# Optimization experiments

Hardware: AMD Instinct MI355X
Metric: run time of the kernel (lower is better)

The kernel has to match this reference:

```python
import jax, jax.numpy as jnp
import numpy as np

IN_F, OUT_F, RANK = 4096, 4096, 16
SCALING = 1.0  # alpha defaults to rank -> alpha/rank == 1.0


def setup_inputs() -> dict:
    key = jax.random.key(0)
    k1, k2, k3, k4 = jax.random.split(key, 4)
    x = jax.random.normal(k1, (4, 2048, IN_F), dtype=jnp.float32)
    base_weight = jax.random.normal(k2, (OUT_F, IN_F), dtype=jnp.float32)
    U = jax.random.normal(k3, (OUT_F, RANK), dtype=jnp.float32)
    s = jnp.ones((RANK,), dtype=jnp.float32)
    V = jax.random.normal(k4, (IN_F, RANK), dtype=jnp.float32)
    return {"x": x, "base_weight": base_weight, "U": U, "s": s, "V": V}


def reference(x, base_weight, U, s, V):
    # delta_weight = scaling * (U * s) @ V^T, shape (out, in)
    delta_w = SCALING * jnp.einsum('or,ir->oi', U * s[None, :], V)
    adapted = base_weight + delta_w
    # x @ adapted^T : (..., in) -> (..., out)
    return jnp.einsum('bsi,oi->bso', x, adapted)
```

## Files before the change

### kernel.cpp

```cpp
#include <hip/hip_runtime.h>


#define IN_F   4096
#define OUT_F  4096
#define RANK   16
#define M_ROWS 8192
#define BM 128
#define BN 128
#define BK 32

typedef _Float16 f16x8 __attribute__((ext_vector_type(8)));
typedef _Float16 f16x4 __attribute__((ext_vector_type(4)));
typedef float    f32x4 __attribute__((ext_vector_type(4)));

__device__ __forceinline__ void async16(const void* gp, void* lp) {
  __builtin_amdgcn_global_load_lds(
      (const __attribute__((address_space(1))) void*)gp,
      (__attribute__((address_space(3))) void*)lp, 16, 0, 0);
}

__global__ void split_x_kernel(const float* __restrict__ x,
                               _Float16* __restrict__ xh) {
  size_t t = (size_t)blockIdx.x * 256 + threadIdx.x;
  float4 v = ((const float4*)x)[t];
  f16x4 h;
  h[0] = (_Float16)v.x; h[1] = (_Float16)v.y;
  h[2] = (_Float16)v.z; h[3] = (_Float16)v.w;
  ((f16x4*)xh)[t] = h;
}

__global__ void prep_w_kernel(const float* __restrict__ W,
                              const float* __restrict__ U,
                              const float* __restrict__ S,
                              const float* __restrict__ V,
                              _Float16* __restrict__ wh) {
  int t = blockIdx.x * 256 + threadIdx.x;
  int i4 = (t & 1023) << 2;
  int o0 = (t >> 10) << 3;

  float v[4][RANK];
#pragma unroll
  for (int j = 0; j < 4; ++j) {
    const float4* vp = (const float4*)(V + (size_t)(i4 + j) * RANK);
#pragma unroll
    for (int q = 0; q < 4; ++q) {
      float4 vv = vp[q];
      v[j][q * 4 + 0] = vv.x; v[j][q * 4 + 1] = vv.y;
      v[j][q * 4 + 2] = vv.z; v[j][q * 4 + 3] = vv.w;
    }
  }
  float sv[RANK];
#pragma unroll
  for (int r = 0; r < RANK; r += 4) {
    float4 ss = *(const float4*)(S + r);
    sv[r] = ss.x; sv[r + 1] = ss.y; sv[r + 2] = ss.z; sv[r + 3] = ss.w;
  }

  for (int oo = 0; oo < 8; ++oo) {
    int o = o0 + oo;
    float us[RANK];
    const float4* up = (const float4*)(U + (size_t)o * RANK);
#pragma unroll
    for (int r = 0; r < RANK; r += 4) {
      float4 uu = up[r >> 2];
      us[r] = uu.x * sv[r]; us[r + 1] = uu.y * sv[r + 1];
      us[r + 2] = uu.z * sv[r + 2]; us[r + 3] = uu.w * sv[r + 3];
    }
    float4 w = *(const float4*)(W + (size_t)o * IN_F + i4);
    float d0 = w.x, d1 = w.y, d2 = w.z, d3 = w.w;
#pragma unroll
    for (int r = 0; r < RANK; ++r) {
      d0 += us[r] * v[0][r];
      d1 += us[r] * v[1][r];
      d2 += us[r] * v[2][r];
      d3 += us[r] * v[3][r];
    }
    f16x4 h;
    h[0] = (_Float16)d0; h[1] = (_Float16)d1;
    h[2] = (_Float16)d2; h[3] = (_Float16)d3;
    *(f16x4*)(wh + (size_t)o * IN_F + i4) = h;
  }
}

__global__ __launch_bounds__(256, 2)
void gemm_kernel(const _Float16* __restrict__ xh,
                 const _Float16* __restrict__ wh,
                 float* __restrict__ out) {
  __shared__ unsigned char lds[16384];

  const int bid = blockIdx.x;
  const int nt = bid & 31;
  const int mt = bid >> 5;
  const int blockM = mt * BM;
  const int blockN = nt * BN;
  const int lane = threadIdx.x & 63;
  const int wave = threadIdx.x >> 6;
  const int wm = wave >> 1, wn = wave & 1;

  const _Float16* gPtr[4];
  unsigned ldsOff[4];
#pragma unroll
  for (int q = 0; q < 4; ++q) {
    int slot = (wave * 4 + q) * 64 + lane;
    int op = slot >> 9;
    int rem = slot & 511;
    int r = rem >> 2;
    int c = rem & 3;
    int cd = c ^ ((r >> 1) & 3);
    const _Float16* base =
        op ? wh + (size_t)(blockN + r) * IN_F
           : xh + (size_t)(blockM + r) * IN_F;
    gPtr[q] = base + cd * 8;
    ldsOff[q] = slot * 16;
  }

  unsigned offA[4], offB[4];
  const int kg = lane >> 4;
#pragma unroll
  for (int t = 0; t < 4; ++t) {
    int mrow = wm * 64 + t * 16 + (lane & 15);
    offA[t] = mrow * 64 + ((kg ^ ((mrow >> 1) & 3)) * 16);
    int nrow = wn * 64 + t * 16 + (lane & 15);
    offB[t] = 8192 + nrow * 64 + ((kg ^ ((nrow >> 1) & 3)) * 16);
  }

  f32x4 acc[4][4];
#pragma unroll
  for (int i = 0; i < 4; ++i)
#pragma unroll
    for (int j = 0; j < 4; ++j) acc[i][j] = (f32x4){0.f, 0.f, 0.f, 0.f};

  for (int kk = 0; kk < IN_F; kk += BK) {
#pragma unroll
    for (int q = 0; q < 4; ++q) async16(gPtr[q] + kk, lds + ldsOff[q]);
    __syncthreads();

    f16x8 aF[4], bF[4];
#pragma unroll
    for (int t = 0; t < 4; ++t) {
      aF[t] = *(const f16x8*)(lds + offA[t]);
      bF[t] = *(const f16x8*)(lds + offB[t]);
    }
    __syncthreads();

#pragma unroll
    for (int i = 0; i < 4; ++i)
#pragma unroll
      for (int j = 0; j < 4; ++j)
        acc[i][j] = __builtin_amdgcn_mfma_f32_16x16x32_f16(aF[i], bF[j], acc[i][j], 0, 0, 0);
  }

  const int col0 = blockN + wn * 64 + (lane & 15);
  const int row0 = blockM + wm * 64 + (lane >> 4) * 4;
#pragma unroll
  for (int i = 0; i < 4; ++i)
#pragma unroll
    for (int j = 0; j < 4; ++j) {
      float* op = out + (size_t)(row0 + i * 16) * OUT_F + col0 + j * 16;
#pragma unroll
      for (int rr = 0; rr < 4; ++rr) op[(size_t)rr * OUT_F] = acc[i][j][rr];
    }
}

__global__ __launch_bounds__(256)
void fb_gemm(const float* __restrict__ x, const float* __restrict__ W,
             float* __restrict__ out) {
  __shared__ float xs[64][17];
  __shared__ float wsm[64][17];
  const int mt = blockIdx.x >> 6;
  const int ntile = blockIdx.x & 63;
  const int bM = mt * 64, bN = ntile * 64;
  const int t = threadIdx.x;
  const int lr = t >> 2, lc = (t & 3) * 4;
  const int tm = t >> 4, tn = t & 15;

  float acc[4][4];
#pragma unroll
  for (int i = 0; i < 4; ++i)
#pragma unroll
    for (int j = 0; j < 4; ++j) acc[i][j] = 0.f;

  for (int kk = 0; kk < IN_F; kk += 16) {
    float4 xa = *(const float4*)(x + (size_t)(bM + lr) * IN_F + kk + lc);
    float4 wa = *(const float4*)(W + (size_t)(bN + lr) * IN_F + kk + lc);
    xs[lr][lc + 0] = xa.x; xs[lr][lc + 1] = xa.y;
    xs[lr][lc + 2] = xa.z; xs[lr][lc + 3] = xa.w;
    wsm[lr][lc + 0] = wa.x; wsm[lr][lc + 1] = wa.y;
    wsm[lr][lc + 2] = wa.z; wsm[lr][lc + 3] = wa.w;
    __syncthreads();
#pragma unroll
    for (int k = 0; k < 16; ++k) {
      float a[4], b[4];
#pragma unroll
      for (int i = 0; i < 4; ++i) a[i] = xs[tm * 4 + i][k];
#pragma unroll
      for (int j = 0; j < 4; ++j) b[j] = wsm[tn * 4 + j][k];
#pragma unroll
      for (int i = 0; i < 4; ++i)
#pragma unroll
        for (int j = 0; j < 4; ++j) acc[i][j] += a[i] * b[j];
    }
    __syncthreads();
  }
#pragma unroll
  for (int i = 0; i < 4; ++i)
#pragma unroll
    for (int j = 0; j < 4; ++j)
      out[(size_t)(bM + tm * 4 + i) * OUT_F + bN + tn * 4 + j] = acc[i][j];
}

__global__ void fb_xv(const float* __restrict__ x, const float* __restrict__ V,
                      const float* __restrict__ S, float* __restrict__ xv) {
  int m = blockIdx.x * 4 + (threadIdx.x >> 6);
  int lane = threadIdx.x & 63;
  float a[RANK];
#pragma unroll
  for (int r = 0; r < RANK; ++r) a[r] = 0.f;
  for (int k = lane; k < IN_F; k += 64) {
    float xe = x[(size_t)m * IN_F + k];
    const float4* vp = (const float4*)(V + (size_t)k * RANK);
#pragma unroll
    for (int q = 0; q < 4; ++q) {
      float4 vv = vp[q];
      a[q * 4 + 0] += xe * vv.x; a[q * 4 + 1] += xe * vv.y;
      a[q * 4 + 2] += xe * vv.z; a[q * 4 + 3] += xe * vv.w;
    }
  }
#pragma unroll
  for (int r = 0; r < RANK; ++r)
    for (int off = 32; off; off >>= 1) a[r] += __shfl_down(a[r], off);
  if (lane == 0) {
#pragma unroll
    for (int r = 0; r < RANK; ++r) xv[(size_t)m * RANK + r] = a[r] * S[r];
  }
}

__global__ void fb_add(const float* __restrict__ xv, const float* __restrict__ U,
                       float* __restrict__ out) {
  size_t t = (size_t)blockIdx.x * 256 + threadIdx.x;
  int m = (int)(t >> 12), o = (int)(t & 4095);
  const float* xr = xv + (size_t)m * RANK;
  const float* ur = U + (size_t)o * RANK;
  float d = 0.f;
#pragma unroll
  for (int r = 0; r < RANK; ++r) d += xr[r] * ur[r];
  out[t] += d;
}

extern "C" void kernel_launch(void* const* d_in, const int* in_sizes, int n_in,
                              void* d_out, int out_size, void* d_ws, size_t ws_size,
                              hipStream_t stream) {
  const float* x = (const float*)d_in[0];
  const float* W = (const float*)d_in[1];
  const float* U = (const float*)d_in[2];
  const float* s = (const float*)d_in[3];
  const float* V = (const float*)d_in[4];
  float* out = (float*)d_out;

  const size_t need = ((size_t)M_ROWS * IN_F + (size_t)OUT_F * IN_F) * 2;
  if (ws_size >= need) {
    _Float16* xh = (_Float16*)d_ws;
    _Float16* wh = xh + (size_t)M_ROWS * IN_F;
    split_x_kernel<<<(M_ROWS * IN_F / 4) / 256, 256, 0, stream>>>(x, xh);
    prep_w_kernel<<<((IN_F / 4) * (OUT_F / 8)) / 256, 256, 0, stream>>>(W, U, s, V, wh);
    gemm_kernel<<<(M_ROWS / BM) * (OUT_F / BN), 256, 0, stream>>>(xh, wh, out);
  } else {
    float* xv = (float*)d_ws;
    fb_gemm<<<(M_ROWS / 64) * (OUT_F / 64), 256, 0, stream>>>(x, W, out);
    fb_xv<<<M_ROWS / 4, 256, 0, stream>>>(x, V, s, xv);
    fb_add<<<(size_t)M_ROWS * OUT_F / 256, 256, 0, stream>>>(xv, U, out);
  }
}
```

Measured before the change: 613.2 us.

## Rewrite GEMM with 256x256 tiles, double-buffered async LDS pipeline, fused prep kernel

Merges the x fp16 conversion and the adapted-weight prep into a single launch. Rewrites the fp16 MFMA GEMM to use 256x256x64 tiles with 512 threads, 128KB of double-buffered LDS, and a software pipeline that issues async global-to-LDS loads two stages ahead and interleaves them with MFMA phases. It also adds an XCD-aware block remap, s_setprio around the MFMA phases, and explicit waitcnt/barrier scheduling. The aim is to hide global load latency and raise arithmetic intensity, in exchange for heavy LDS use (128KB per block, so the launch bound of 2 blocks per CU is likely unreachable) and fragile hand-tuned synchronisation.

```diff
diff --git a/kernel.cpp b/kernel.cpp
--- a/kernel.cpp
+++ b/kernel.cpp
@@ -5,9 +5,10 @@
 #define OUT_F  4096
 #define RANK   16
 #define M_ROWS 8192
-#define BM 128
-#define BN 128
-#define BK 32
+#define BM 256
+#define BN 256
+#define BK 64
+#define NT (IN_F / BK)
 
 typedef _Float16 f16x8 __attribute__((ext_vector_type(8)));
 typedef _Float16 f16x4 __attribute__((ext_vector_type(4)));
@@ -19,141 +20,232 @@
       (__attribute__((address_space(3))) void*)lp, 16, 0, 0);
 }
 
-__global__ void split_x_kernel(const float* __restrict__ x,
-                               _Float16* __restrict__ xh) {
-  size_t t = (size_t)blockIdx.x * 256 + threadIdx.x;
-  float4 v = ((const float4*)x)[t];
-  f16x4 h;
-  h[0] = (_Float16)v.x; h[1] = (_Float16)v.y;
-  h[2] = (_Float16)v.z; h[3] = (_Float16)v.w;
-  ((f16x4*)xh)[t] = h;
-}
-
-__global__ void prep_w_kernel(const float* __restrict__ W,
-                              const float* __restrict__ U,
-                              const float* __restrict__ S,
-                              const float* __restrict__ V,
-                              _Float16* __restrict__ wh) {
-  int t = blockIdx.x * 256 + threadIdx.x;
-  int i4 = (t & 1023) << 2;
-  int o0 = (t >> 10) << 3;
-
-  float v[4][RANK];
-#pragma unroll
-  for (int j = 0; j < 4; ++j) {
-    const float4* vp = (const float4*)(V + (size_t)(i4 + j) * RANK);
-#pragma unroll
-    for (int q = 0; q < 4; ++q) {
-      float4 vv = vp[q];
-      v[j][q * 4 + 0] = vv.x; v[j][q * 4 + 1] = vv.y;
-      v[j][q * 4 + 2] = vv.z; v[j][q * 4 + 3] = vv.w;
-    }
-  }
-  float sv[RANK];
-#pragma unroll
-  for (int r = 0; r < RANK; r += 4) {
-    float4 ss = *(const float4*)(S + r);
-    sv[r] = ss.x; sv[r + 1] = ss.y; sv[r + 2] = ss.z; sv[r + 3] = ss.w;
-  }
-
-  for (int oo = 0; oo < 8; ++oo) {
-    int o = o0 + oo;
-    float us[RANK];
-    const float4* up = (const float4*)(U + (size_t)o * RANK);
+#define SPLIT_BLOCKS 4096
+
+__global__ __launch_bounds__(256)
+void prep_kernel(const float* __restrict__ x, _Float16* __restrict__ xh,
+                 const float* __restrict__ W, const float* __restrict__ U,
+                 const float* __restrict__ S, const float* __restrict__ V,
+                 _Float16* __restrict__ wh) {
+  if (blockIdx.x < SPLIT_BLOCKS) {
+    size_t t = (size_t)blockIdx.x * 256 + threadIdx.x;
+#pragma unroll
+    for (int it = 0; it < 8; ++it) {
+      float4 v = ((const float4*)x)[t];
+      f16x4 h;
+      h[0] = (_Float16)v.x; h[1] = (_Float16)v.y;
+      h[2] = (_Float16)v.z; h[3] = (_Float16)v.w;
+      ((f16x4*)xh)[t] = h;
+      t += (size_t)SPLIT_BLOCKS * 256;
+    }
+  } else {
+    int t = (int)(blockIdx.x - SPLIT_BLOCKS) * 256 + threadIdx.x;
+    int i4 = (t & 1023) << 2;
+    int o0 = (t >> 10) << 3;
+
+    float v[4][RANK];
+#pragma unroll
+    for (int j = 0; j < 4; ++j) {
+      const float4* vp = (const float4*)(V + (size_t)(i4 + j) * RANK);
+#pragma unroll
+      for (int q = 0; q < 4; ++q) {
+        float4 vv = vp[q];
+        v[j][q * 4 + 0] = vv.x; v[j][q * 4 + 1] = vv.y;
+        v[j][q * 4 + 2] = vv.z; v[j][q * 4 + 3] = vv.w;
+      }
+    }
+    float sv[RANK];
 #pragma unroll
     for (int r = 0; r < RANK; r += 4) {
-      float4 uu = up[r >> 2];
-      us[r] = uu.x * sv[r]; us[r + 1] = uu.y * sv[r + 1];
-      us[r + 2] = uu.z * sv[r + 2]; us[r + 3] = uu.w * sv[r + 3];
-    }
-    float4 w = *(const float4*)(W + (size_t)o * IN_F + i4);
-    float d0 = w.x, d1 = w.y, d2 = w.z, d3 = w.w;
-#pragma unroll
-    for (int r = 0; r < RANK; ++r) {
-      d0 += us[r] * v[0][r];
-      d1 += us[r] * v[1][r];
-      d2 += us[r] * v[2][r];
-      d3 += us[r] * v[3][r];
-    }
-    f16x4 h;
-    h[0] = (_Float16)d0; h[1] = (_Float16)d1;
-    h[2] = (_Float16)d2; h[3] = (_Float16)d3;
-    *(f16x4*)(wh + (size_t)o * IN_F + i4) = h;
-  }
-}
-
-__global__ __launch_bounds__(256, 2)
+      float4 ss = *(const float4*)(S + r);
+      sv[r] = ss.x; sv[r + 1] = ss.y; sv[r + 2] = ss.z; sv[r + 3] = ss.w;
+    }
+
+    for (int oo = 0; oo < 8; ++oo) {
+      int o = o0 + oo;
+      float us[RANK];
+      const float4* up = (const float4*)(U + (size_t)o * RANK);
+#pragma unroll
+      for (int r = 0; r < RANK; r += 4) {
+        float4 uu = up[r >> 2];
+        us[r] = uu.x * sv[r]; us[r + 1] = uu.y * sv[r + 1];
+        us[r + 2] = uu.z * sv[r + 2]; us[r + 3] = uu.w * sv[r + 3];
+      }
+      float4 w = *(const float4*)(W + (size_t)o * IN_F + i4);
+      float d0 = w.x, d1 = w.y, d2 = w.z, d3 = w.w;
+#pragma unroll
+      for (int r = 0; r < RANK; ++r) {
+        d0 += us[r] * v[0][r];
+        d1 += us[r] * v[1][r];
+        d2 += us[r] * v[2][r];
+        d3 += us[r] * v[3][r];
+      }
+      f16x4 h;
+      h[0] = (_Float16)d0; h[1] = (_Float16)d1;
+      h[2] = (_Float16)d2; h[3] = (_Float16)d3;
+      *(f16x4*)(wh + (size_t)o * IN_F + i4) = h;
+    }
+  }
+}
+
+__global__ __launch_bounds__(512, 2)
 void gemm_kernel(const _Float16* __restrict__ xh,
                  const _Float16* __restrict__ wh,
                  float* __restrict__ out) {
-  __shared__ unsigned char lds[16384];
-
-  const int bid = blockIdx.x;
-  const int nt = bid & 31;
-  const int mt = bid >> 5;
+  __shared__ unsigned char lds[131072];
+
+  const int orig = blockIdx.x;
+  const int wg = (orig & 7) * 64 + (orig >> 3);
+  const int mt = wg >> 4;
+  const int nt = wg & 15;
   const int blockM = mt * BM;
   const int blockN = nt * BN;
-  const int lane = threadIdx.x & 63;
-  const int wave = threadIdx.x >> 6;
-  const int wm = wave >> 1, wn = wave & 1;
-
-  const _Float16* gPtr[4];
-  unsigned ldsOff[4];
-#pragma unroll
-  for (int q = 0; q < 4; ++q) {
-    int slot = (wave * 4 + q) * 64 + lane;
-    int op = slot >> 9;
-    int rem = slot & 511;
-    int r = rem >> 2;
-    int c = rem & 3;
+
+  const int tid = threadIdx.x;
+  const int lane = tid & 63;
+  const int wave = tid >> 6;
+  const int wm = wave >> 2;
+  const int wn = wave & 3;
+
+  const _Float16* aSrc[2];
+  const _Float16* bSrc[2];
+  unsigned ldsOff[2];
+#pragma unroll
+  for (int q = 0; q < 2; ++q) {
+    int slot = q * 512 + tid;
+    int r = slot >> 2;
+    int c = slot & 3;
     int cd = c ^ ((r >> 1) & 3);
-    const _Float16* base =
-        op ? wh + (size_t)(blockN + r) * IN_F
-           : xh + (size_t)(blockM + r) * IN_F;
-    gPtr[q] = base + cd * 8;
-    ldsOff[q] = slot * 16;
-  }
-
+    aSrc[q] = xh + (size_t)(blockM + r) * IN_F + cd * 8;
+    bSrc[q] = wh + (size_t)(blockN + r) * IN_F + cd * 8;
+    ldsOff[q] = (unsigned)slot * 16;
+  }
+
+  const int kg = lane >> 4;
   unsigned offA[4], offB[4];
-  const int kg = lane >> 4;
 #pragma unroll
   for (int t = 0; t < 4; ++t) {
-    int mrow = wm * 64 + t * 16 + (lane & 15);
-    offA[t] = mrow * 64 + ((kg ^ ((mrow >> 1) & 3)) * 16);
-    int nrow = wn * 64 + t * 16 + (lane & 15);
-    offB[t] = 8192 + nrow * 64 + ((kg ^ ((nrow >> 1) & 3)) * 16);
-  }
-
-  f32x4 acc[4][4];
-#pragma unroll
-  for (int i = 0; i < 4; ++i)
+    int ar = wm * 128 + t * 16 + (lane & 15);
+    offA[t] = (unsigned)(ar * 64 + ((kg ^ ((ar >> 1) & 3)) * 16));
+    int br = wn * 64 + t * 16 + (lane & 15);
+    offB[t] = (unsigned)(br * 64 + ((kg ^ ((br >> 1) & 3)) * 16));
+  }
+
+  f32x4 acc[8][4];
+#pragma unroll
+  for (int i = 0; i < 8; ++i)
 #pragma unroll
     for (int j = 0; j < 4; ++j) acc[i][j] = (f32x4){0.f, 0.f, 0.f, 0.f};
 
-  for (int kk = 0; kk < IN_F; kk += BK) {
-#pragma unroll
-    for (int q = 0; q < 4; ++q) async16(gPtr[q] + kk, lds + ldsOff[q]);
-    __syncthreads();
+#define STG(SRC, LDSBASE, KOFS)                                      \
+  {                                                                  \
+    async16(SRC[0] + (KOFS), lds + (LDSBASE) + ldsOff[0]);           \
+    async16(SRC[1] + (KOFS), lds + (LDSBASE) + ldsOff[1]);           \
+  }
+
+  STG(aSrc, 0, 0);
+  STG(bSrc, 16384, 0);
+  STG(aSrc, 32768, 32);
+  STG(bSrc, 49152, 32);
+  STG(bSrc, 65536 + 16384, 64);
+  STG(aSrc, 65536 + 0, 64);
+  STG(bSrc, 65536 + 49152, 96);
+  asm volatile("s_waitcnt vmcnt(6)" ::: "memory");
+  __builtin_amdgcn_s_barrier();
+
+#pragma unroll 2
+  for (int t = 0; t < NT; ++t) {
+    const unsigned base = (unsigned)(t & 1) << 16;
+    const unsigned baseN = base ^ 65536u;
+    const int kof1 = (t + 1) * BK;
+    const int kof2 = (t + 2) * BK;
+    const bool ok1 = (t + 1) < NT;
+    const bool ok2 = (t + 2) < NT;
+
+    if (t >= NT - 2) {
+      asm volatile("s_waitcnt vmcnt(0)" ::: "memory");
+      __builtin_amdgcn_s_barrier();
+    }
 
     f16x8 aF[4], bF[4];
-#pragma unroll
-    for (int t = 0; t < 4; ++t) {
-      aF[t] = *(const f16x8*)(lds + offA[t]);
-      bF[t] = *(const f16x8*)(lds + offB[t]);
-    }
-    __syncthreads();
-
+
+#pragma unroll
+    for (int i = 0; i < 4; ++i)
+      aF[i] = *(const f16x8*)(lds + base + offA[i]);
+#pragma unroll
+    for (int j = 0; j < 4; ++j)
+      bF[j] = *(const f16x8*)(lds + base + 16384 + offB[j]);
+    if (ok1) STG(aSrc, baseN + 32768, kof1 + 32);
+    __builtin_amdgcn_s_barrier();
+    asm volatile("s_waitcnt lgkmcnt(0)" ::: "memory");
+    __builtin_amdgcn_sched_barrier(0);
+    __builtin_amdgcn_s_setprio(1);
 #pragma unroll
     for (int i = 0; i < 4; ++i)
 #pragma unroll
       for (int j = 0; j < 4; ++j)
         acc[i][j] = __builtin_amdgcn_mfma_f32_16x16x32_f16(aF[i], bF[j], acc[i][j], 0, 0, 0);
-  }
+    __builtin_amdgcn_s_setprio(0);
+    __builtin_amdgcn_s_barrier();
+
+#pragma unroll
+    for (int i = 0; i < 4; ++i)
+      aF[i] = *(const f16x8*)(lds + base + 4096 + offA[i]);
+    if (ok2) STG(bSrc, base + 16384, kof2);
+    __builtin_amdgcn_s_barrier();
+    asm volatile("s_waitcnt lgkmcnt(0)" ::: "memory");
+    __builtin_amdgcn_sched_barrier(0);
+    __builtin_amdgcn_s_setprio(1);
+#pragma unroll
+    for (int i = 0; i < 4; ++i)
+#pragma unroll
+      for (int j = 0; j < 4; ++j)
+        acc[4 + i][j] = __builtin_amdgcn_mfma_f32_16x16x32_f16(aF[i], bF[j], acc[4 + i][j], 0, 0, 0);
+    __builtin_amdgcn_s_setprio(0);
+    __builtin_amdgcn_s_barrier();
+
+#pragma unroll
+    for (int i = 0; i < 4; ++i)
+      aF[i] = *(const f16x8*)(lds + base + 32768 + offA[i]);
+#pragma unroll
+    for (int j = 0; j < 4; ++j)
+      bF[j] = *(const f16x8*)(lds + base + 49152 + offB[j]);
+    if (ok2) STG(aSrc, base + 0, kof2);
+    __builtin_amdgcn_s_barrier();
+    asm volatile("s_waitcnt lgkmcnt(0)" ::: "memory");
+    __builtin_amdgcn_sched_barrier(0);
+    __builtin_amdgcn_s_setprio(1);
+#pragma unroll
+    for (int i = 0; i < 4; ++i)
+#pragma unroll
+      for (int j = 0; j < 4; ++j)
+        acc[i][j] = __builtin_amdgcn_mfma_f32_16x16x32_f16(aF[i], bF[j], acc[i][j], 0, 0, 0);
+    __builtin_amdgcn_s_setprio(0);
+    __builtin_amdgcn_s_barrier();
+
+#pragma unroll
+    for (int i = 0; i < 4; ++i)
+      aF[i] = *(const f16x8*)(lds + base + 32768 + 4096 + offA[i]);
+    if (ok2) STG(bSrc, base + 49152, kof2 + 32);
+    asm volatile("s_waitcnt vmcnt(6)" ::: "memory");
+    __builtin_amdgcn_s_barrier();
+    asm volatile("s_waitcnt lgkmcnt(0)" ::: "memory");
+    __builtin_amdgcn_sched_barrier(0);
+    __builtin_amdgcn_s_setprio(1);
+#pragma unroll
+    for (int i = 0; i < 4; ++i)
+#pragma unroll
+      for (int j = 0; j < 4; ++j)
+        acc[4 + i][j] = __builtin_amdgcn_mfma_f32_16x16x32_f16(aF[i], bF[j], acc[4 + i][j], 0, 0, 0);
+    __builtin_amdgcn_s_setprio(0);
+    __builtin_amdgcn_s_barrier();
+  }
+#undef STG
 
   const int col0 = blockN + wn * 64 + (lane & 15);
-  const int row0 = blockM + wm * 64 + (lane >> 4) * 4;
-#pragma unroll
-  for (int i = 0; i < 4; ++i)
+  const int row0 = blockM + wm * 128 + (lane >> 4) * 4;
+#pragma unroll
+  for (int i = 0; i < 8; ++i)
 #pragma unroll
     for (int j = 0; j < 4; ++j) {
       float* op = out + (size_t)(row0 + i * 16) * OUT_F + col0 + j * 16;
@@ -261,9 +353,9 @@
   if (ws_size >= need) {
     _Float16* xh = (_Float16*)d_ws;
     _Float16* wh = xh + (size_t)M_ROWS * IN_F;
-    split_x_kernel<<<(M_ROWS * IN_F / 4) / 256, 256, 0, stream>>>(x, xh);
-    prep_w_kernel<<<((IN_F / 4) * (OUT_F / 8)) / 256, 256, 0, stream>>>(W, U, s, V, wh);
-    gemm_kernel<<<(M_ROWS / BM) * (OUT_F / BN), 256, 0, stream>>>(xh, wh, out);
+    prep_kernel<<<SPLIT_BLOCKS + ((IN_F / 4) * (OUT_F / 8)) / 256, 256, 0, stream>>>(
+        x, xh, W, U, s, V, wh);
+    gemm_kernel<<<(M_ROWS / BM) * (OUT_F / BN), 512, 0, stream>>>(xh, wh, out);
   } else {
     float* xv = (float*)d_ws;
     fb_gemm<<<(M_ROWS / 64) * (OUT_F / 64), 256, 0, stream>>>(x, W, out);
```

Result: faster. 545.5 us (-11.0%).
